# Kernel tuning notes

Measured on AMD Instinct MI355X. Metric: run time of the kernel, lower is better.

The kernel has to match this reference:

```python
import jax, jax.numpy as jnp
import numpy as np


def _cd2(a, b):
    # squared euclidean distances [n,m]
    d = jnp.sum(a * a, 1)[:, None] + jnp.sum(b * b, 1)[None, :] - 2.0 * (a @ b.T)
    return jnp.maximum(d, 0.0)


def _cdist(a, b):
    # tiny clamp keeps sqrt grad finite on the zero diagonal, fwd unchanged
    return jnp.sqrt(jnp.maximum(_cd2(a, b), 1e-30))


def _tmedian(x):
    # torch.median semantics: lower middle element
    f = jnp.sort(x.reshape(-1))
    return f[(f.shape[0] - 1) // 2]


def setup_inputs() -> dict:
    key = jax.random.key(0)
    k1, k2 = jax.random.split(key)
    feat_s = jax.random.normal(k1, (25, 640), dtype=jnp.float32)
    y_s = (jnp.arange(25) % 5).astype(jnp.int32)  # 5-way 5-shot, every class present
    feat_q = jax.random.normal(k2, (300, 640), dtype=jnp.float32)
    return {"feat_s": feat_s, "y_s": y_s, "feat_q": feat_q}


def reference(feat_s, y_s, feat_q):
    y_s_np = np.asarray(y_s)
    classes = np.unique(y_s_np)
    C = int(classes.shape[0])
    onehot = jnp.asarray(y_s_np[:, None] == classes[None, :], dtype=feat_s.dtype)  # [S,C]
    prototypes = (onehot.T @ feat_s) / jnp.sum(onehot, 0)[:, None]  # [C,D]

    # ---- virtual mixup densification ----
    dist_q = _cdist(feat_q, prototypes)  # [Nq,C]
    y_boot = np.asarray(jnp.argmin(dist_q, 1))
    q_norm = feat_q / jnp.linalg.norm(feat_q, axis=1, keepdims=True)
    cos_np = np.asarray(q_norm @ q_norm.T)
    dist_q_np = np.asarray(dist_q)
    virt = []
    for c in range(C):
        idx = np.flatnonzero(y_boot == c)
        if idx.size < 2:
            continue
        cos_c = cos_np[np.ix_(idx, idx)]
        f = np.sort(cos_c.reshape(-1))
        thresh = f[(f.size - 1) // 2]  # torch lower median
        ii, jj = np.nonzero(np.triu(cos_c >= thresh, 1))  # pairs with i<j
        if ii.size:
            virt.append(0.5 * (feat_q[idx[ii]] + feat_q[idx[jj]]))
        kq = int(idx[np.argmin(dist_q_np[idx, c])])
        virt.append((0.5 * (prototypes[c] + feat_q[kq]))[None, :])
    feat_all = jnp.concatenate([feat_q] + virt, 0) if virt else feat_q

    # ---- self-tuning affinity (kNN graph) ----
    n = int(feat_all.shape[0])
    k = max(1, int(np.log2(n)))
    dist = _cdist(feat_all, feat_all)  # [n,n]
    _, nn_idx = jax.lax.top_k(-dist, k + 1)  # smallest k+1 (incl. self)
    sigma = dist[jnp.arange(n), nn_idx[:, k]] + 1e-8
    nbrs = nn_idx[:, 1:]  # [n,k]
    d_nb = jnp.take_along_axis(dist, nbrs, 1)
    w = jnp.exp(-d_nb / (sigma[:, None] * sigma[nbrs]))
    W = jnp.zeros((n, n), feat_all.dtype).at[jnp.arange(n)[:, None], nbrs].set(w)
    W = (W + W.T) / 2
    D_inv = 1.0 / (W.sum(1) + 1e-8)

    # ---- density-adaptive lambda ----
    d = _cdist(feat_all, prototypes).min(1)
    lam = jnp.exp(-(d ** 2) / (2 * _tmedian(d) ** 2 + 1e-8))

    # ---- mm iterations (label propagation) ----
    a = _cd2(feat_all, prototypes)  # [n,C]
    y0 = jax.nn.softmax(-a, axis=1)
    scale = (lam * D_inv)[:, None]

    def step(carry, _):
        y, done = carry
        y_new = jax.nn.softmax(-a + scale * (W @ y), axis=1)
        conv = jnp.max(jnp.abs(y_new - y)) < 1e-4
        y_out = jnp.where(done | conv, y, y_new)  # emulate torch early break
        return (y_out, done | conv), None

    (y, _), _ = jax.lax.scan(step, (y0, jnp.asarray(False)), None, length=50)
    preds = jnp.argmax(y[: feat_q.shape[0]], 1)
    return preds
```

## Files before the change

kernel.cpp:

```cpp
#include <hip/hip_runtime.h>
#include <math.h>

#define CMAX 8
#define KMAX 16
#define TPB 256
#define BNMAX 1024

struct P {
  const float* fs; const int* ys; const float* fq;
  int S, Q, D, BN, NMAX;
  float* proto;
  float* G;
  float* cosq;
  int* ybt;
  int* cls; int* scount; int* qcount; int* qidx; int* kq;
  float* thr;
  int* rowcnt; int* rowoff; int* paircnt; int* basev;
  int* meta;
  int* uv;
  float* rn2;
  int* cand;
  int* nbrs; float* dnb; float* wgt; float* sigma;
  int* indeg; int* inoff; int* cursor;
  int* insrcU; float* inwU; int* indst;
  int* insrc; float* inw;
  unsigned* cosk;
  unsigned* gmaxu;
  float* amat; float* dinv; float* dmin; float* scalev;
  float* yA; float* yB;
  float* meddenom;
  int* outp;
};

__device__ inline unsigned f2key(float f){
  unsigned b=__float_as_uint(f);
  return (b&0x80000000u)? ~b : (b|0x80000000u);
}
__device__ inline float key2f(unsigned k){
  unsigned b=(k&0x80000000u)? (k^0x80000000u) : ~k;
  return __uint_as_float(b);
}
__device__ inline unsigned long long shfl_xor_u64(unsigned long long v,int m){
  unsigned lo=(unsigned)v, hi=(unsigned)(v>>32);
  lo=__shfl_xor(lo,m,64); hi=__shfl_xor(hi,m,64);
  return (((unsigned long long)hi)<<32)|lo;
}

__global__ void k_init(P p){
  if (threadIdx.x==0){
    int labs[CMAX]; int cnt[CMAX]; int C=0;
    for (int s=0;s<p.S;s++){
      int l=p.ys[s]; int f=-1;
      for(int c=0;c<C;c++) if(labs[c]==l){f=c;break;}
      if(f<0){ if(C<CMAX){labs[C]=l;cnt[C]=1;C++;} }
      else cnt[f]++;
    }
    for(int a=0;a<C;a++)for(int b=a+1;b<C;b++)
      if(labs[b]<labs[a]){int t=labs[a];labs[a]=labs[b];labs[b]=t;
                          t=cnt[a];cnt[a]=cnt[b];cnt[b]=t;}
    for(int c=0;c<C;c++){p.cls[c]=labs[c];p.scount[c]=cnt[c];}
    p.meta[0]=C;
  }
}

__global__ void k_proto(P p){
  int c=blockIdx.x; int C=p.meta[0];
  for(int d=threadIdx.x; d<p.D; d+=blockDim.x){
    float s=0.f;
    if(c<C){
      int lab=p.cls[c];
      for(int j=0;j<p.S;j++) if(p.ys[j]==lab) s+=p.fs[(size_t)j*p.D+d];
      s/= (float)p.scount[c];
    }
    p.proto[(size_t)c*p.D+d]=s;
  }
}

__global__ void k_gram(P p){
  __shared__ float arow[1024];
  int a=blockIdx.x;
  const float* ra = (a<p.Q)? p.fq + (size_t)a*p.D : p.proto + (size_t)(a-p.Q)*p.D;
  const float* A = ra;
  if(p.D<=1024){
    for(int d=threadIdx.x; d<p.D; d+=blockDim.x) arow[d]=ra[d];
    __syncthreads();
    A=(const float*)arow;
  }
  int D4=p.D>>2; int Dt=D4<<2;
  for(int b=threadIdx.x; b<p.BN; b+=blockDim.x){
    const float* rb=(b<p.Q)? p.fq+(size_t)b*p.D : p.proto+(size_t)(b-p.Q)*p.D;
    const float4* a4=(const float4*)A;
    const float4* b4=(const float4*)rb;
    float s=0.f;
    #pragma unroll 4
    for(int d=0;d<D4;d++){
      float4 x=a4[d], y=b4[d];
      s += x.x*y.x + x.y*y.y + x.z*y.z + x.w*y.w;
    }
    for(int d=Dt;d<p.D;d++) s += A[d]*rb[d];
    p.G[(size_t)a*p.BN+b]=s;
  }
}

__global__ void k_cos(P p){
  int t=blockIdx.x*blockDim.x+threadIdx.x;
  if(t>=p.Q*p.Q)return;
  int i=t/p.Q, j=t%p.Q;
  p.cosq[t]=p.G[(size_t)i*p.BN+j]/(sqrtf(p.G[(size_t)i*p.BN+i])*sqrtf(p.G[(size_t)j*p.BN+j]));
}

__global__ void k_yboot(P p){
  int q=blockIdx.x*blockDim.x+threadIdx.x;
  if(q>=p.Q)return;
  int C=p.meta[0];
  float gq=p.G[(size_t)q*p.BN+q];
  float best=INFINITY; int bc=0;
  for(int c=0;c<C;c++){
    int pc=p.Q+c;
    float d2=gq+p.G[(size_t)pc*p.BN+pc]-2.f*p.G[(size_t)q*p.BN+pc];
    d2=fmaxf(d2,0.f);
    if(d2<best){best=d2;bc=c;}
  }
  p.ybt[q]=bc;
}

__global__ void k_qidx(P p){
  int c=blockIdx.x; int C=p.meta[0];
  int lane=threadIdx.x;
  if(c>=C){ if(lane==0){p.qcount[c]=0;p.kq[c]=0;} return; }
  int base=0;
  for(int q0=0;q0<p.Q;q0+=64){
    int q=q0+lane;
    bool in = (q<p.Q) && (p.ybt[q]==c);
    unsigned long long mask=__ballot(in);
    int pre=__popcll(mask & ((lane==63)?0x7FFFFFFFFFFFFFFFull:((1ull<<lane)-1ull)));
    if(in) p.qidx[c*p.Q+base+pre]=q;
    base+=__popcll(mask);
  }
  if(lane==0) p.qcount[c]=base;
  int pc=p.Q+c;
  float gp=p.G[(size_t)pc*p.BN+pc];
  unsigned long long best=0xFFFFFFFFFFFFFFFFull;
  for(int t=lane;t<base;t+=64){
    int q=p.qidx[c*p.Q+t];
    float d2=fmaxf(p.G[(size_t)q*p.BN+q]+gp-2.f*p.G[(size_t)q*p.BN+pc],0.f);
    unsigned long long key=(((unsigned long long)f2key(d2))<<32)|(unsigned)t;
    if(key<best)best=key;
  }
  #pragma unroll
  for(int s=32;s>=1;s>>=1){
    unsigned long long o=shfl_xor_u64(best,s);
    if(o<best)best=o;
  }
  if(lane==0){
    int t=(int)(unsigned)(best&0xFFFFFFFFull);
    p.kq[c]=(base>0)? p.qidx[c*p.Q+t] : 0;
  }
}

__global__ void k_median(P p){
  __shared__ unsigned hist[256];
  __shared__ unsigned sPref; __shared__ int sTrem;
  __shared__ int sqidx[512];
  int c=blockIdx.x; int C=p.meta[0];
  int m=(c<C)? p.qcount[c]:0;
  int tid=threadIdx.x;
  if(m<2){ if(tid==0) p.thr[c]=INFINITY; return; }
  const int* qix;
  if(p.Q<=512){
    for(int t=tid;t<m;t+=blockDim.x) sqidx[t]=p.qidx[c*p.Q+t];
    __syncthreads();
    qix=sqidx;
  } else qix=p.qidx+c*p.Q;
  int total=m*m;
  unsigned* keys=p.cosk+(size_t)c*p.Q*p.Q;
  for(int t=tid;t<total;t+=blockDim.x){
    int a=t/m, b=t-a*m;
    keys[t]=f2key(p.cosq[(size_t)qix[a]*p.Q+qix[b]]);
  }
  if(tid==0){ sPref=0u; sTrem=(total-1)/2; }
  __syncthreads();
  unsigned prefmask=0u;
  for(int shift=24;shift>=0;shift-=8){
    hist[tid&255]=0u;
    __syncthreads();
    unsigned pref=sPref;
    for(int t=tid;t<total;t+=blockDim.x){
      unsigned key=keys[t];
      if((key&prefmask)==pref) atomicAdd(&hist[(key>>shift)&255],1u);
    }
    __syncthreads();
    if(tid==0){
      int trem=sTrem; unsigned cum=0;
      for(int b=0;b<256;b++){
        unsigned h=hist[b];
        if(cum+h>(unsigned)trem){ sPref=pref|((unsigned)b<<shift); sTrem=trem-(int)cum; break; }
        cum+=h;
      }
    }
    __syncthreads();
    prefmask|=(0xFFu<<shift);
  }
  if(tid==0) p.thr[c]=key2f(sPref);
}

__global__ void k_rowcnt(P p){
  int c=blockIdx.x; int C=p.meta[0];
  int m=(c<C)? p.qcount[c]:0;
  if(m<2){ if(threadIdx.x==0) p.paircnt[c]=0; return; }
  float th=p.thr[c];
  for(int a=threadIdx.x;a<m;a+=blockDim.x){
    int ia=p.qidx[c*p.Q+a]; int cnt=0;
    const float* row=p.cosq+(size_t)ia*p.Q;
    for(int b=a+1;b<m;b++){
      int ib=p.qidx[c*p.Q+b];
      cnt += (row[ib]>=th);
    }
    p.rowcnt[c*p.Q+a]=cnt;
  }
  __syncthreads();
  if(threadIdx.x==0){
    int run=0;
    for(int a=0;a<m;a++){p.rowoff[c*p.Q+a]=run; run+=p.rowcnt[c*p.Q+a];}
    p.paircnt[c]=run;
  }
}

__global__ void k_bases(P p){
  int C=p.meta[0]; int cur=p.Q;
  for(int c=0;c<C;c++){
    p.basev[c]=cur;
    if(p.qcount[c]>=2) cur += p.paircnt[c]+1;
  }
  int n=cur; if(n>p.NMAX)n=p.NMAX;
  p.meta[1]=n;
  int k=31-__clz(n); if(k<1)k=1; if(k>KMAX-1)k=KMAX-1;
  p.meta[2]=k;
  p.meta[3]=0;
  p.meta[4]=0;
  p.meta[5]=0;
  for(int t=0;t<64;t++) p.gmaxu[t]=0u;
}

__global__ void k_uv(P p){
  int r=blockIdx.x*blockDim.x+threadIdx.x;
  if(r>=p.NMAX)return;
  p.indeg[r]=0;
  if(r<p.Q){ p.uv[2*r]=r; p.uv[2*r+1]=r; }
}

__global__ void k_uvpairs(P p){
  int c=blockIdx.x; int C=p.meta[0];
  int m=(c<C)? p.qcount[c]:0;
  if(m<2)return;
  float th=p.thr[c];
  int bs=p.basev[c];
  for(int a=threadIdx.x;a<m;a+=blockDim.x){
    int ia=p.qidx[c*p.Q+a];
    int off=bs+p.rowoff[c*p.Q+a]; int cnt=0;
    const float* row=p.cosq+(size_t)ia*p.Q;
    for(int b=a+1;b<m;b++){
      int ib=p.qidx[c*p.Q+b];
      if(row[ib]>=th){
        int r=off+cnt;
        p.uv[2*r]=ia; p.uv[2*r+1]=ib;
        cnt++;
      }
    }
  }
  if(threadIdx.x==0){
    int r=bs+p.paircnt[c];
    p.uv[2*r]=p.Q+c; p.uv[2*r+1]=p.kq[c];
  }
}

__global__ void k_rn2c(P p){
  int r=blockIdx.x*blockDim.x+threadIdx.x;
  int n=p.meta[1]; if(r>=n)return;
  int u=p.uv[2*r],v=p.uv[2*r+1];
  float hu=0.5f*(p.G[(size_t)u*p.BN+u]+p.G[(size_t)v*p.BN+u]);
  float hv=0.5f*(p.G[(size_t)u*p.BN+v]+p.G[(size_t)v*p.BN+v]);
  float rn=0.5f*(hu+hv);
  p.rn2[r]=rn;
  ((int4*)p.cand)[r]=make_int4(u,v,__float_as_int(rn),0);
}

template<int KSEL>
__device__ void knn_scan(const P& p,int n,int kp1,const float* sh,bool useSh,
                         const float* Gu,const float* Gv,float rni,
                         unsigned long long* wl){
  int lane=threadIdx.x&63; int w=threadIdx.x>>6;
  unsigned kf[KSEL]; int kj[KSEL];
  #pragma unroll
  for(int t=0;t<KSEL;t++){ kf[t]=0xFFFFFFFFu; kj[t]=0x7FFFFFFF; }
  unsigned thrw=0xFFFFFFFFu;
  int iters=(n+127)>>7;
  const int4* cand=(const int4*)p.cand;
  for(int it=0;it<iters;++it){
    int j=(it<<7)+(w<<6)+lane;
    unsigned key=0xFFFFFFFFu;
    if(j<n){
      int4 cd=cand[j];
      float dot = useSh ? (sh[cd.x]+sh[cd.y])
                        : 0.5f*(Gu[cd.x]+Gv[cd.x])+0.5f*(Gu[cd.y]+Gv[cd.y]);
      float d2=fmaxf(rni+__int_as_float(cd.z)-dot,0.f);
      key=f2key(d2);
    }
    if(key<=thrw && key<kf[KSEL-1]){
      int cj=j;
      #pragma unroll
      for(int t=0;t<KSEL;t++){
        bool lt = key<kf[t];
        unsigned nk = lt? key : kf[t];
        unsigned ok = lt? kf[t] : key;
        int nj = lt? cj : kj[t];
        int oj = lt? kj[t] : cj;
        kf[t]=nk; kj[t]=nj; key=ok; cj=oj;
      }
    }
    if((it&7)==7){
      unsigned v=kf[KSEL-1];
      #pragma unroll
      for(int s=32;s>=1;s>>=1){
        unsigned o=(unsigned)__shfl_xor((int)v,s,64);
        if(o<v)v=o;
      }
      thrw=v;
    }
  }
  for(int t=0;t<kp1;t++){
    unsigned long long mv=(((unsigned long long)kf[0])<<32)|(unsigned)kj[0];
    unsigned long long m=mv;
    #pragma unroll
    for(int s=32;s>=1;s>>=1){
      unsigned long long o=shfl_xor_u64(m,s);
      if(o<m)m=o;
    }
    if(mv==m){
      #pragma unroll
      for(int q=0;q<KSEL-1;q++){ kf[q]=kf[q+1]; kj[q]=kj[q+1]; }
      kf[KSEL-1]=0xFFFFFFFFu; kj[KSEL-1]=0x7FFFFFFF;
    }
    if(lane==0) wl[w*16+t]=m;
  }
}

__global__ void __launch_bounds__(128) k_knn(P p){
  __shared__ float sh[BNMAX];
  __shared__ unsigned long long wl[32];
  int i=blockIdx.x;
  int n=p.meta[1]; if(i>=n)return;
  int kp1=p.meta[2]+1;
  int u1=p.uv[2*i], v1=p.uv[2*i+1];
  const float* Gu=p.G+(size_t)u1*p.BN;
  const float* Gv=p.G+(size_t)v1*p.BN;
  bool useSh=(p.BN<=BNMAX);
  if(useSh){
    for(int d=threadIdx.x; d<p.BN; d+=128) sh[d]=0.5f*(Gu[d]+Gv[d]);
  }
  __syncthreads();
  float rni=p.rn2[i];
  if(kp1<=13) knn_scan<13>(p,n,kp1,sh,useSh,Gu,Gv,rni,wl);
  else        knn_scan<16>(p,n,kp1,sh,useSh,Gu,Gv,rni,wl);
  __syncthreads();
  if(threadIdx.x==0){
    int a=0,b=0;
    for(int t=0;t<kp1;t++){
      unsigned long long va=wl[a], vb=wl[16+b];
      unsigned long long m;
      if(va<=vb){m=va;a++;} else {m=vb;b++;}
      int j=(int)(unsigned)(m&0xFFFFFFFFull);
      float d2=key2f((unsigned)(m>>32));
      float dd=sqrtf(fmaxf(d2,1e-30f));
      if(t>=1){ p.nbrs[(size_t)i*KMAX+t-1]=j; p.dnb[(size_t)i*KMAX+t-1]=dd; }
      if(t==kp1-1) p.sigma[i]=dd+1e-8f;
    }
  }
}

__global__ void k_wgtcnt(P p){
  int i=blockIdx.x*blockDim.x+threadIdx.x;
  int n=p.meta[1]; if(i>=n)return;
  int k=p.meta[2];
  float si=p.sigma[i];
  for(int q=0;q<k;q++){
    int j=p.nbrs[(size_t)i*KMAX+q];
    p.wgt[(size_t)i*KMAX+q]=expf(-p.dnb[(size_t)i*KMAX+q]/(si*p.sigma[j]));
    atomicAdd(&p.indeg[j],1);
  }
  for(int q=k;q<KMAX;q++){ p.nbrs[(size_t)i*KMAX+q]=i; p.wgt[(size_t)i*KMAX+q]=0.f; }
}

__global__ void k_scan(P p){
  __shared__ int part[TPB];
  int n=p.meta[1];
  int chunk=(n+TPB-1)/TPB;
  int beg=threadIdx.x*chunk, end=beg+chunk; if(end>n)end=n;
  int s=0;
  for(int i=beg;i<end;i++) s+=p.indeg[i];
  part[threadIdx.x]=s; __syncthreads();
  if(threadIdx.x==0){
    int run=0;
    for(int t=0;t<TPB;t++){int v=part[t];part[t]=run;run+=v;}
    p.inoff[n]=run;
  }
  __syncthreads();
  int run=part[threadIdx.x];
  for(int i=beg;i<end;i++){
    p.inoff[i]=run; p.cursor[i]=run; run+=p.indeg[i];
  }
}

__global__ void k_fill(P p){
  int i=blockIdx.x*blockDim.x+threadIdx.x;
  int n=p.meta[1]; if(i>=n)return;
  int k=p.meta[2];
  for(int q=0;q<k;q++){
    int dst=p.nbrs[(size_t)i*KMAX+q];
    int slot=atomicAdd(&p.cursor[dst],1);
    p.insrcU[slot]=i; p.inwU[slot]=p.wgt[(size_t)i*KMAX+q]; p.indst[slot]=dst;
  }
}

__global__ void k_rank(P p){
  int e=blockIdx.x*blockDim.x+threadIdx.x;
  int n=p.meta[1];
  int E=p.inoff[n];
  if(e>=E)return;
  int dst=p.indst[e];
  int b=p.inoff[dst], en=p.inoff[dst+1];
  int s=p.insrcU[e]; float w=p.inwU[e];
  int rank=0;
  for(int x=b;x<en;x++) rank += (p.insrcU[x]<s);
  p.insrc[b+rank]=s; p.inw[b+rank]=w;
}

__global__ void k_dad(P p){
  int i=blockIdx.x*blockDim.x+threadIdx.x;
  int n=p.meta[1]; if(i>=n)return;
  int k=p.meta[2]; int C=p.meta[0];
  float s=0.f;
  for(int q=0;q<k;q++) s+=p.wgt[(size_t)i*KMAX+q];
  for(int e=p.inoff[i];e<p.inoff[i+1];e++) s+=p.inw[e];
  p.dinv[i]=1.f/(0.5f*s+1e-8f);
  int u=p.uv[2*i],v=p.uv[2*i+1];
  float rn=p.rn2[i]; float mn=INFINITY;
  #pragma unroll
  for(int c=0;c<CMAX;c++){
    float a=INFINITY;
    if(c<C){
      int pc=p.Q+c;
      a=rn+p.G[(size_t)pc*p.BN+pc]-(p.G[(size_t)u*p.BN+pc]+p.G[(size_t)v*p.BN+pc]);
      a=fmaxf(a,0.f);
      mn=fminf(mn,a);
    }
    p.amat[(size_t)i*CMAX+c]=a;
  }
  p.dmin[i]=sqrtf(fmaxf(mn,1e-30f));
}

__global__ void k_medd(P p){
  __shared__ unsigned hist[256];
  __shared__ unsigned sPref; __shared__ int sTrem;
  int n=p.meta[1];
  int tid=threadIdx.x;
  if(tid==0){ sPref=0u; sTrem=(n-1)/2; }
  __syncthreads();
  unsigned prefmask=0u;
  for(int shift=24;shift>=0;shift-=8){
    hist[tid&255]=0u;
    __syncthreads();
    unsigned pref=sPref;
    for(int i=tid;i<n;i+=blockDim.x){
      unsigned key=f2key(p.dmin[i]);
      if((key&prefmask)==pref) atomicAdd(&hist[(key>>shift)&255],1u);
    }
    __syncthreads();
    if(tid==0){
      int trem=sTrem; unsigned cum=0;
      for(int b=0;b<256;b++){
        unsigned h=hist[b];
        if(cum+h>(unsigned)trem){ sPref=pref|((unsigned)b<<shift); sTrem=trem-(int)cum; break; }
        cum+=h;
      }
    }
    __syncthreads();
    prefmask|=(0xFFu<<shift);
  }
  if(tid==0){
    float med=key2f(sPref);
    p.meddenom[0]=2.f*med*med+1e-8f;
  }
}

__global__ void k_y0(P p){
  int i=blockIdx.x*blockDim.x+threadIdx.x;
  int n=p.meta[1]; if(i>=n)return;
  float la=expf(-(p.dmin[i]*p.dmin[i])/p.meddenom[0]);
  p.scalev[i]=la*p.dinv[i];
  float mn=INFINITY;
  #pragma unroll
  for(int c=0;c<CMAX;c++) mn=fminf(mn,p.amat[(size_t)i*CMAX+c]);
  float ex[CMAX]; float sum=0.f;
  #pragma unroll
  for(int c=0;c<CMAX;c++){
    float e=expf(mn-p.amat[(size_t)i*CMAX+c]);
    ex[c]=e; sum+=e;
  }
  float inv=1.f/sum;
  #pragma unroll
  for(int c=0;c<CMAX;c++) p.yA[(size_t)i*CMAX+c]=ex[c]*inv;
}

__global__ void __launch_bounds__(256) k_step(P p,int t){
  if(p.meta[3]) return;
  int n=p.meta[1];
  int par=p.meta[4];
  float* cur=par? p.yB : p.yA;
  float* nxt=par? p.yA : p.yB;
  int gt=blockIdx.x*blockDim.x+threadIdx.x;
  int i=gt>>2; int sub=gt&3;
  float dmx=0.f;
  if(i<n){
    float wax=0,way=0,waz=0,waw=0,wbx=0,wby=0,wbz=0,wbw=0;
    #pragma unroll
    for(int m=0;m<4;m++){
      int q=sub+4*m;
      int j=p.nbrs[(size_t)i*KMAX+q];
      float w=p.wgt[(size_t)i*KMAX+q];
      const float4* yr=(const float4*)(cur+(size_t)j*CMAX);
      float4 y0=yr[0],y1=yr[1];
      wax+=w*y0.x; way+=w*y0.y; waz+=w*y0.z; waw+=w*y0.w;
      wbx+=w*y1.x; wby+=w*y1.y; wbz+=w*y1.z; wbw+=w*y1.w;
    }
    int e1=p.inoff[i+1];
    for(int e=p.inoff[i]+sub;e<e1;e+=4){
      int j=p.insrc[e]; float w=p.inw[e];
      const float4* yr=(const float4*)(cur+(size_t)j*CMAX);
      float4 y0=yr[0],y1=yr[1];
      wax+=w*y0.x; way+=w*y0.y; waz+=w*y0.z; waw+=w*y0.w;
      wbx+=w*y1.x; wby+=w*y1.y; wbz+=w*y1.z; wbw+=w*y1.w;
    }
    #pragma unroll
    for(int m=1;m<=2;m<<=1){
      wax+=__shfl_xor(wax,m,64); way+=__shfl_xor(way,m,64);
      waz+=__shfl_xor(waz,m,64); waw+=__shfl_xor(waw,m,64);
      wbx+=__shfl_xor(wbx,m,64); wby+=__shfl_xor(wby,m,64);
      wbz+=__shfl_xor(wbz,m,64); wbw+=__shfl_xor(wbw,m,64);
    }
    float sc=p.scalev[i]*0.5f;
    const float4* am=(const float4*)(p.amat+(size_t)i*CMAX);
    float4 a0=am[0],a1=am[1];
    float l0=sc*wax-a0.x, l1=sc*way-a0.y, l2=sc*waz-a0.z, l3=sc*waw-a0.w;
    float l4=sc*wbx-a1.x, l5=sc*wby-a1.y, l6=sc*wbz-a1.z, l7=sc*wbw-a1.w;
    float mx=fmaxf(fmaxf(fmaxf(l0,l1),fmaxf(l2,l3)),fmaxf(fmaxf(l4,l5),fmaxf(l6,l7)));
    float x0=expf(l0-mx),x1=expf(l1-mx),x2=expf(l2-mx),x3=expf(l3-mx);
    float x4=expf(l4-mx),x5=expf(l5-mx),x6=expf(l6-mx),x7=expf(l7-mx);
    float inv=1.f/(x0+x1+x2+x3+x4+x5+x6+x7);
    float4 o0=make_float4(x0*inv,x1*inv,x2*inv,x3*inv);
    float4 o1=make_float4(x4*inv,x5*inv,x6*inv,x7*inv);
    if(sub==0){
      const float4* cr=(const float4*)(cur+(size_t)i*CMAX);
      float4 c0=cr[0],c1=cr[1];
      dmx=fmaxf(dmx,fabsf(o0.x-c0.x)); dmx=fmaxf(dmx,fabsf(o0.y-c0.y));
      dmx=fmaxf(dmx,fabsf(o0.z-c0.z)); dmx=fmaxf(dmx,fabsf(o0.w-c0.w));
      dmx=fmaxf(dmx,fabsf(o1.x-c1.x)); dmx=fmaxf(dmx,fabsf(o1.y-c1.y));
      dmx=fmaxf(dmx,fabsf(o1.z-c1.z)); dmx=fmaxf(dmx,fabsf(o1.w-c1.w));
      float4* nr=(float4*)(nxt+(size_t)i*CMAX);
      nr[0]=o0; nr[1]=o1;
    }
  }
  #pragma unroll
  for(int s=32;s>=1;s>>=1) dmx=fmaxf(dmx,__shfl_xor(dmx,s,64));
  if((threadIdx.x&63)==0) atomicMax(p.gmaxu+t,__float_as_uint(dmx));
  __syncthreads();
  if(threadIdx.x==0){
    __threadfence();
    int fin=atomicAdd(&p.meta[5],1);
    if(fin==(int)gridDim.x-1){
      p.meta[5]=0;
      float mm=__uint_as_float(p.gmaxu[t]);
      if(mm<1e-4f) p.meta[3]=1;
      else         p.meta[4]=par^1;
    }
  }
}

__global__ void k_arg(P p){
  int q=blockIdx.x*blockDim.x+threadIdx.x;
  if(q>=p.Q)return;
  int C=p.meta[0];
  const float* cur=p.meta[4]? p.yB : p.yA;
  float best=cur[(size_t)q*CMAX+0]; int bc=0;
  for(int c=1;c<C;c++){
    float v=cur[(size_t)q*CMAX+c];
    if(v>best){best=v;bc=c;}
  }
  p.outp[q]=bc;
}


static void make_layout(char* base,int S,int Q,int D,int BN,long N,
                        const float*fs,const int*ys,const float*fq,
                        int* outp, P* pp, size_t* need){
  size_t off=0;
  auto A=[&](size_t b)->char*{
    size_t o=(off+255)&~(size_t)255; off=o+b; return base+o;
  };
  P p{};
  p.fs=fs;p.ys=ys;p.fq=fq;p.S=S;p.Q=Q;p.D=D;p.BN=BN;p.NMAX=(int)N;
  p.proto=(float*)A(4ul*CMAX*D);
  p.G=(float*)A(4ul*(size_t)BN*BN);
  p.cosq=(float*)A(4ul*(size_t)Q*Q);
  p.ybt=(int*)A(4ul*Q);
  p.cls=(int*)A(4ul*CMAX);
  p.scount=(int*)A(4ul*CMAX);
  p.qcount=(int*)A(4ul*CMAX);
  p.qidx=(int*)A(4ul*CMAX*Q);
  p.kq=(int*)A(4ul*CMAX);
  p.thr=(float*)A(4ul*CMAX);
  p.rowcnt=(int*)A(4ul*CMAX*Q);
  p.rowoff=(int*)A(4ul*CMAX*Q);
  p.paircnt=(int*)A(4ul*CMAX);
  p.basev=(int*)A(4ul*CMAX);
  p.meta=(int*)A(4ul*16);
  p.uv=(int*)A(8ul*N);
  p.rn2=(float*)A(4ul*N);
  p.cand=(int*)A(16ul*N);
  p.nbrs=(int*)A(4ul*KMAX*N);
  p.dnb=(float*)A(4ul*KMAX*N);
  p.wgt=(float*)A(4ul*KMAX*N);
  p.sigma=(float*)A(4ul*N);
  p.indeg=(int*)A(4ul*N);
  p.inoff=(int*)A(4ul*(N+1));
  p.cursor=(int*)A(4ul*N);
  p.insrcU=(int*)A(4ul*KMAX*N);
  p.inwU=(float*)A(4ul*KMAX*N);
  p.indst=(int*)A(4ul*KMAX*N);
  p.insrc=(int*)A(4ul*KMAX*N);
  p.inw=(float*)A(4ul*KMAX*N);
  p.cosk=(unsigned*)A(4ul*CMAX*(size_t)Q*Q);
  p.gmaxu=(unsigned*)A(4ul*64);
  p.amat=(float*)A(4ul*CMAX*N);
  p.dinv=(float*)A(4ul*N);
  p.dmin=(float*)A(4ul*N);
  p.scalev=(float*)A(4ul*N);
  p.yA=(float*)A(4ul*CMAX*N);
  p.yB=(float*)A(4ul*CMAX*N);
  p.meddenom=(float*)A(4ul*4);
  p.outp=outp;
  *pp=p; *need=off;
}

extern "C" void kernel_launch(void* const* d_in, const int* in_sizes, int n_in,
                              void* d_out, int out_size, void* d_ws, size_t ws_size,
                              hipStream_t stream){
  const float* fs=(const float*)d_in[0];
  const int*   ys=(const int*)d_in[1];
  const float* fq=(const float*)d_in[2];
  int S=in_sizes[1];
  int D=in_sizes[0]/S;
  int Q=in_sizes[2]/D;
  int BN=Q+CMAX;

  long full=(long)Q + (long)Q*(Q-1)/2 + CMAX;
  long cand[4]={full,16384,8192,5000};
  P p{}; size_t need=0; int NMAX=(int)cand[3];
  for(int ci=0;ci<4;ci++){
    long N=cand[ci]; if(N<Q+CMAX)N=Q+CMAX;
    make_layout((char*)d_ws,S,Q,D,BN,N,fs,ys,fq,(int*)d_out,&p,&need);
    NMAX=(int)N;
    if(need<=ws_size) break;
  }

  int gN=(NMAX+TPB-1)/TPB;
  long gEl=((long)NMAX*KMAX+TPB-1)/TPB;
  int gE=(int)gEl;
  int gS=(NMAX+63)/64;

  k_init   <<<1, 64, 0, stream>>>(p);
  k_proto  <<<CMAX, TPB, 0, stream>>>(p);
  k_gram   <<<BN, TPB, 0, stream>>>(p);
  k_cos    <<<(Q*Q+TPB-1)/TPB, TPB, 0, stream>>>(p);
  k_yboot  <<<(Q+TPB-1)/TPB, TPB, 0, stream>>>(p);
  k_qidx   <<<CMAX, 64, 0, stream>>>(p);
  k_median <<<CMAX, TPB, 0, stream>>>(p);
  k_rowcnt <<<CMAX, TPB, 0, stream>>>(p);
  k_bases  <<<1, 1, 0, stream>>>(p);
  k_uv     <<<gN, TPB, 0, stream>>>(p);
  k_uvpairs<<<CMAX, TPB, 0, stream>>>(p);
  k_rn2c   <<<gN, TPB, 0, stream>>>(p);
  k_knn    <<<NMAX, 128, 0, stream>>>(p);
  k_wgtcnt <<<gN, TPB, 0, stream>>>(p);
  k_scan   <<<1, TPB, 0, stream>>>(p);
  k_fill   <<<gN, TPB, 0, stream>>>(p);
  k_rank   <<<gE, TPB, 0, stream>>>(p);
  k_dad    <<<gN, TPB, 0, stream>>>(p);
  k_medd   <<<1, TPB, 0, stream>>>(p);
  k_y0     <<<gN, TPB, 0, stream>>>(p);
  for(int t=0;t<50;t++)
    k_step <<<gS, 256, 0, stream>>>(p, t);
  k_arg    <<<(Q+TPB-1)/TPB, TPB, 0, stream>>>(p);
}
```

Before: 604.4 us.

## Store every label-propagation iterate and pick the converged one at the end

```diff
diff --git a/kernel.cpp b/kernel.cpp
--- a/kernel.cpp
+++ b/kernel.cpp
@@ -5,6 +5,7 @@
 #define KMAX 16
 #define TPB 256
 #define BNMAX 1024
+#define NSTEP 50
 
 struct P {
   const float* fs; const int* ys; const float* fq;
@@ -12,7 +13,6 @@
   float* proto;
   float* G;
   float* cosq;
-  int* ybt;
   int* cls; int* scount; int* qcount; int* qidx; int* kq;
   float* thr;
   int* rowcnt; int* rowoff; int* paircnt; int* basev;
@@ -23,11 +23,11 @@
   int* nbrs; float* dnb; float* wgt; float* sigma;
   int* indeg; int* inoff; int* cursor;
   int* insrcU; float* inwU; int* indst;
-  int* insrc; float* inw;
+  int2* inedge;
   unsigned* cosk;
   unsigned* gmaxu;
   float* amat; float* dinv; float* dmin; float* scalev;
-  float* yA; float* yB;
+  float* ybufs;
   float* meddenom;
   int* outp;
 };
@@ -109,21 +109,6 @@
   p.cosq[t]=p.G[(size_t)i*p.BN+j]/(sqrtf(p.G[(size_t)i*p.BN+i])*sqrtf(p.G[(size_t)j*p.BN+j]));
 }
 
-__global__ void k_yboot(P p){
-  int q=blockIdx.x*blockDim.x+threadIdx.x;
-  if(q>=p.Q)return;
-  int C=p.meta[0];
-  float gq=p.G[(size_t)q*p.BN+q];
-  float best=INFINITY; int bc=0;
-  for(int c=0;c<C;c++){
-    int pc=p.Q+c;
-    float d2=gq+p.G[(size_t)pc*p.BN+pc]-2.f*p.G[(size_t)q*p.BN+pc];
-    d2=fmaxf(d2,0.f);
-    if(d2<best){best=d2;bc=c;}
-  }
-  p.ybt[q]=bc;
-}
-
 __global__ void k_qidx(P p){
   int c=blockIdx.x; int C=p.meta[0];
   int lane=threadIdx.x;
@@ -131,7 +116,17 @@
   int base=0;
   for(int q0=0;q0<p.Q;q0+=64){
     int q=q0+lane;
-    bool in = (q<p.Q) && (p.ybt[q]==c);
+    bool in=false;
+    if(q<p.Q){
+      float gq=p.G[(size_t)q*p.BN+q];
+      float best=INFINITY; int bc=0;
+      for(int cc=0;cc<C;cc++){
+        int pc=p.Q+cc;
+        float d2=fmaxf(gq+p.G[(size_t)pc*p.BN+pc]-2.f*p.G[(size_t)q*p.BN+pc],0.f);
+        if(d2<best){best=d2;bc=cc;}
+      }
+      in=(bc==c);
+    }
     unsigned long long mask=__ballot(in);
     int pre=__popcll(mask & ((lane==63)?0x7FFFFFFFFFFFFFFFull:((1ull<<lane)-1ull)));
     if(in) p.qidx[c*p.Q+base+pre]=q;
@@ -236,9 +231,6 @@
   p.meta[1]=n;
   int k=31-__clz(n); if(k<1)k=1; if(k>KMAX-1)k=KMAX-1;
   p.meta[2]=k;
-  p.meta[3]=0;
-  p.meta[4]=0;
-  p.meta[5]=0;
   for(int t=0;t<64;t++) p.gmaxu[t]=0u;
 }
 
@@ -304,7 +296,7 @@
       float dot = useSh ? (sh[cd.x]+sh[cd.y])
                         : 0.5f*(Gu[cd.x]+Gv[cd.x])+0.5f*(Gu[cd.y]+Gv[cd.y]);
       float d2=fmaxf(rni+__int_as_float(cd.z)-dot,0.f);
-      key=f2key(d2);
+      key=__float_as_uint(d2);
     }
     if(key<=thrw && key<kf[KSEL-1]){
       int cj=j;
@@ -370,7 +362,7 @@
       unsigned long long m;
       if(va<=vb){m=va;a++;} else {m=vb;b++;}
       int j=(int)(unsigned)(m&0xFFFFFFFFull);
-      float d2=key2f((unsigned)(m>>32));
+      float d2=__uint_as_float((unsigned)(m>>32));
       float dd=sqrtf(fmaxf(d2,1e-30f));
       if(t>=1){ p.nbrs[(size_t)i*KMAX+t-1]=j; p.dnb[(size_t)i*KMAX+t-1]=dd; }
       if(t==kp1-1) p.sigma[i]=dd+1e-8f;
@@ -432,7 +424,7 @@
   int s=p.insrcU[e]; float w=p.inwU[e];
   int rank=0;
   for(int x=b;x<en;x++) rank += (p.insrcU[x]<s);
-  p.insrc[b+rank]=s; p.inw[b+rank]=w;
+  p.inedge[b+rank]=make_int2(s,__float_as_int(w));
 }
 
 __global__ void k_dad(P p){
@@ -441,7 +433,7 @@
   int k=p.meta[2]; int C=p.meta[0];
   float s=0.f;
   for(int q=0;q<k;q++) s+=p.wgt[(size_t)i*KMAX+q];
-  for(int e=p.inoff[i];e<p.inoff[i+1];e++) s+=p.inw[e];
+  for(int e=p.inoff[i];e<p.inoff[i+1];e++) s+=__int_as_float(p.inedge[e].y);
   p.dinv[i]=1.f/(0.5f*s+1e-8f);
   int u=p.uv[2*i],v=p.uv[2*i+1];
   float rn=p.rn2[i]; float mn=INFINITY;
@@ -509,23 +501,20 @@
   }
   float inv=1.f/sum;
   #pragma unroll
-  for(int c=0;c<CMAX;c++) p.yA[(size_t)i*CMAX+c]=ex[c]*inv;
-}
-
-__global__ void __launch_bounds__(256) k_step(P p,int t){
-  if(p.meta[3]) return;
+  for(int c=0;c<CMAX;c++) p.ybufs[(size_t)i*CMAX+c]=ex[c]*inv;
+}
+
+__global__ void __launch_bounds__(64) k_step(P p,int t){
   int n=p.meta[1];
-  int par=p.meta[4];
-  float* cur=par? p.yB : p.yA;
-  float* nxt=par? p.yA : p.yB;
-  int gt=blockIdx.x*blockDim.x+threadIdx.x;
-  int i=gt>>2; int sub=gt&3;
+  size_t st=(size_t)p.NMAX*CMAX;
+  const float* cur=p.ybufs+(size_t)t*st;
+  float*       nxt=p.ybufs+(size_t)(t+1)*st;
+  int i=blockIdx.x*blockDim.x+threadIdx.x;
   float dmx=0.f;
   if(i<n){
     float wax=0,way=0,waz=0,waw=0,wbx=0,wby=0,wbz=0,wbw=0;
     #pragma unroll
-    for(int m=0;m<4;m++){
-      int q=sub+4*m;
+    for(int q=0;q<KMAX;q++){
       int j=p.nbrs[(size_t)i*KMAX+q];
       float w=p.wgt[(size_t)i*KMAX+q];
       const float4* yr=(const float4*)(cur+(size_t)j*CMAX);
@@ -534,19 +523,13 @@
       wbx+=w*y1.x; wby+=w*y1.y; wbz+=w*y1.z; wbw+=w*y1.w;
     }
     int e1=p.inoff[i+1];
-    for(int e=p.inoff[i]+sub;e<e1;e+=4){
-      int j=p.insrc[e]; float w=p.inw[e];
+    for(int e=p.inoff[i];e<e1;e++){
+      int2 e2=p.inedge[e];
+      int j=e2.x; float w=__int_as_float(e2.y);
       const float4* yr=(const float4*)(cur+(size_t)j*CMAX);
       float4 y0=yr[0],y1=yr[1];
       wax+=w*y0.x; way+=w*y0.y; waz+=w*y0.z; waw+=w*y0.w;
       wbx+=w*y1.x; wby+=w*y1.y; wbz+=w*y1.z; wbw+=w*y1.w;
-    }
-    #pragma unroll
-    for(int m=1;m<=2;m<<=1){
-      wax+=__shfl_xor(wax,m,64); way+=__shfl_xor(way,m,64);
-      waz+=__shfl_xor(waz,m,64); waw+=__shfl_xor(waw,m,64);
-      wbx+=__shfl_xor(wbx,m,64); wby+=__shfl_xor(wby,m,64);
-      wbz+=__shfl_xor(wbz,m,64); wbw+=__shfl_xor(wbw,m,64);
     }
     float sc=p.scalev[i]*0.5f;
     const float4* am=(const float4*)(p.amat+(size_t)i*CMAX);
@@ -559,38 +542,35 @@
     float inv=1.f/(x0+x1+x2+x3+x4+x5+x6+x7);
     float4 o0=make_float4(x0*inv,x1*inv,x2*inv,x3*inv);
     float4 o1=make_float4(x4*inv,x5*inv,x6*inv,x7*inv);
-    if(sub==0){
-      const float4* cr=(const float4*)(cur+(size_t)i*CMAX);
-      float4 c0=cr[0],c1=cr[1];
-      dmx=fmaxf(dmx,fabsf(o0.x-c0.x)); dmx=fmaxf(dmx,fabsf(o0.y-c0.y));
-      dmx=fmaxf(dmx,fabsf(o0.z-c0.z)); dmx=fmaxf(dmx,fabsf(o0.w-c0.w));
-      dmx=fmaxf(dmx,fabsf(o1.x-c1.x)); dmx=fmaxf(dmx,fabsf(o1.y-c1.y));
-      dmx=fmaxf(dmx,fabsf(o1.z-c1.z)); dmx=fmaxf(dmx,fabsf(o1.w-c1.w));
-      float4* nr=(float4*)(nxt+(size_t)i*CMAX);
-      nr[0]=o0; nr[1]=o1;
-    }
+    const float4* cr=(const float4*)(cur+(size_t)i*CMAX);
+    float4 c0=cr[0],c1=cr[1];
+    dmx=fmaxf(dmx,fabsf(o0.x-c0.x)); dmx=fmaxf(dmx,fabsf(o0.y-c0.y));
+    dmx=fmaxf(dmx,fabsf(o0.z-c0.z)); dmx=fmaxf(dmx,fabsf(o0.w-c0.w));
+    dmx=fmaxf(dmx,fabsf(o1.x-c1.x)); dmx=fmaxf(dmx,fabsf(o1.y-c1.y));
+    dmx=fmaxf(dmx,fabsf(o1.z-c1.z)); dmx=fmaxf(dmx,fabsf(o1.w-c1.w));
+    float4* nr=(float4*)(nxt+(size_t)i*CMAX);
+    nr[0]=o0; nr[1]=o1;
   }
   #pragma unroll
   for(int s=32;s>=1;s>>=1) dmx=fmaxf(dmx,__shfl_xor(dmx,s,64));
-  if((threadIdx.x&63)==0) atomicMax(p.gmaxu+t,__float_as_uint(dmx));
+  if(threadIdx.x==0)
+    atomicMax(p.gmaxu+t,__float_as_uint(dmx));
+}
+
+__global__ void k_arg(P p){
+  __shared__ int sT;
+  if(threadIdx.x==0){
+    int tsel=NSTEP;
+    for(int t=0;t<NSTEP;t++){
+      if(__uint_as_float(p.gmaxu[t])<1e-4f){ tsel=t; break; }
+    }
+    sT=tsel;
+  }
   __syncthreads();
-  if(threadIdx.x==0){
-    __threadfence();
-    int fin=atomicAdd(&p.meta[5],1);
-    if(fin==(int)gridDim.x-1){
-      p.meta[5]=0;
-      float mm=__uint_as_float(p.gmaxu[t]);
-      if(mm<1e-4f) p.meta[3]=1;
-      else         p.meta[4]=par^1;
-    }
-  }
-}
-
-__global__ void k_arg(P p){
   int q=blockIdx.x*blockDim.x+threadIdx.x;
   if(q>=p.Q)return;
   int C=p.meta[0];
-  const float* cur=p.meta[4]? p.yB : p.yA;
+  const float* cur=p.ybufs+(size_t)sT*(size_t)p.NMAX*CMAX;
   float best=cur[(size_t)q*CMAX+0]; int bc=0;
   for(int c=1;c<C;c++){
     float v=cur[(size_t)q*CMAX+c];
@@ -612,7 +592,6 @@
   p.proto=(float*)A(4ul*CMAX*D);
   p.G=(float*)A(4ul*(size_t)BN*BN);
   p.cosq=(float*)A(4ul*(size_t)Q*Q);
-  p.ybt=(int*)A(4ul*Q);
   p.cls=(int*)A(4ul*CMAX);
   p.scount=(int*)A(4ul*CMAX);
   p.qcount=(int*)A(4ul*CMAX);
@@ -637,16 +616,14 @@
   p.insrcU=(int*)A(4ul*KMAX*N);
   p.inwU=(float*)A(4ul*KMAX*N);
   p.indst=(int*)A(4ul*KMAX*N);
-  p.insrc=(int*)A(4ul*KMAX*N);
-  p.inw=(float*)A(4ul*KMAX*N);
+  p.inedge=(int2*)A(8ul*KMAX*N);
   p.cosk=(unsigned*)A(4ul*CMAX*(size_t)Q*Q);
   p.gmaxu=(unsigned*)A(4ul*64);
   p.amat=(float*)A(4ul*CMAX*N);
   p.dinv=(float*)A(4ul*N);
   p.dmin=(float*)A(4ul*N);
   p.scalev=(float*)A(4ul*N);
-  p.yA=(float*)A(4ul*CMAX*N);
-  p.yB=(float*)A(4ul*CMAX*N);
+  p.ybufs=(float*)A(4ul*CMAX*(size_t)N*(NSTEP+1));
   p.meddenom=(float*)A(4ul*4);
   p.outp=outp;
   *pp=p; *need=off;
@@ -682,7 +659,6 @@
   k_proto  <<<CMAX, TPB, 0, stream>>>(p);
   k_gram   <<<BN, TPB, 0, stream>>>(p);
   k_cos    <<<(Q*Q+TPB-1)/TPB, TPB, 0, stream>>>(p);
-  k_yboot  <<<(Q+TPB-1)/TPB, TPB, 0, stream>>>(p);
   k_qidx   <<<CMAX, 64, 0, stream>>>(p);
   k_median <<<CMAX, TPB, 0, stream>>>(p);
   k_rowcnt <<<CMAX, TPB, 0, stream>>>(p);
@@ -698,7 +674,7 @@
   k_dad    <<<gN, TPB, 0, stream>>>(p);
   k_medd   <<<1, TPB, 0, stream>>>(p);
   k_y0     <<<gN, TPB, 0, stream>>>(p);
-  for(int t=0;t<50;t++)
-    k_step <<<gS, 256, 0, stream>>>(p, t);
+  for(int t=0;t<NSTEP;t++)
+    k_step <<<gS, 64, 0, stream>>>(p, t);
   k_arg    <<<(Q+TPB-1)/TPB, TPB, 0, stream>>>(p);
 }
```

Result: slower. 1.358 ms (+124.7%).
